# Kernel optimization log

Measured on AMD Instinct MI355X. Metric: run time of the kernel, lower is better.

## Reference

```python
import jax, jax.numpy as jnp
import numpy as np

NEG = -1e30  # safe -inf surrogate for log-space DP
BLANK = 0


def _ctc_loss_mean(log_probs, targets):
    """CTC loss matching torch.nn.functional.ctc_loss with reduction='mean',
    blank=0, full input lengths, and fixed target lengths L.
    log_probs: [T, B, C] (treated as log-probabilities, as F.ctc_loss does)
    targets:   [B, L] int labels in [1, C)
    """
    T, B, C = log_probs.shape
    L = targets.shape[1]
    S = 2 * L + 1  # extended label sequence: blank-interleaved

    # ext[b] = [blank, t1, blank, t2, blank]
    ext = jnp.zeros((B, S), dtype=targets.dtype).at[:, 1::2].set(targets)

    # lp_ext[t, b, s] = log_probs[t, b, ext[b, s]]
    lp_ext = jnp.take_along_axis(log_probs, jnp.broadcast_to(ext[None], (T, B, S)), axis=2)

    # transition s-2 -> s allowed only for non-blank states with distinct labels
    skip = jnp.concatenate(
        [jnp.zeros((B, 2), dtype=bool),
         (ext[:, 2:] != BLANK) & (ext[:, 2:] != ext[:, :-2])], axis=1)

    alpha0 = jnp.full((B, S), NEG, log_probs.dtype)
    alpha0 = alpha0.at[:, 0].set(lp_ext[0, :, 0]).at[:, 1].set(lp_ext[0, :, 1])

    neg1 = jnp.full((B, 1), NEG, log_probs.dtype)
    neg2 = jnp.full((B, 2), NEG, log_probs.dtype)

    def step(alpha, lp_t):
        p1 = jnp.concatenate([neg1, alpha[:, :-1]], axis=1)
        p2 = jnp.where(skip, jnp.concatenate([neg2, alpha[:, :-2]], axis=1), NEG)
        alpha_new = lp_t + jax.nn.logsumexp(jnp.stack([alpha, p1, p2]), axis=0)
        return alpha_new, None

    alphaT, _ = jax.lax.scan(step, alpha0, lp_ext[1:])  # scan over t = 1..T-1

    # path ends in last blank or last label
    log_lik = jax.nn.logsumexp(alphaT[:, S - 2:S], axis=1)  # [B]
    # torch 'mean': divide each loss by its target length, then batch mean
    return jnp.mean(-log_lik / L)


def setup_inputs() -> dict:
    T, B, C, L = 512, 32, 8000, 2
    key = jax.random.key(0)
    k1, k2, k3 = jax.random.split(key, 3)
    logit = jax.random.normal(k1, (T, B, C), dtype=jnp.float32)
    label = jax.random.randint(k2, (B, L), 0, C, dtype=jnp.int64)     # unused by forward
    targets = jax.random.randint(k3, (B, L), 1, 20, dtype=jnp.int64)  # torch.randint(1, 20, (B, 2))
    return {"logit": logit, "label": label, "targets": targets}


def reference(logit, label, targets):
    # The torch module ignores `label` and builds random length-2 targets;
    # we receive those as the deterministic `targets` input.
    return _ctc_loss_mean(logit, targets)
```

## Files before the change

kernel.cpp:

```cpp
#include <hip/hip_runtime.h>

#define TT 512
#define BB 32
#define CC 8000
#define LOG2E 1.4426950408889634f
#define LN2   0.6931471805599453f
#define NBLK  8

#if __has_builtin(__builtin_amdgcn_exp2f)
#define EXP2F(x) __builtin_amdgcn_exp2f(x)
#else
#define EXP2F(x) exp2f(x)
#endif
#if __has_builtin(__builtin_amdgcn_logf)
#define LOG2F(x) __builtin_amdgcn_logf(x)
#else
#define LOG2F(x) log2f(x)
#endif

#define WS_CNT_OFF (65 * 512 * 4)

__device__ __forceinline__ void triprod(const float a[15], const float b[15],
                                        float p[15]) {
    p[ 0] = a[0] * b[0];
    p[ 1] = fmaf(a[0], b[ 1], a[1] * b[ 5]);
    p[ 2] = fmaf(a[0], b[ 2], fmaf(a[1], b[ 6], a[2] * b[ 9]));
    p[ 3] = fmaf(a[0], b[ 3], fmaf(a[1], b[ 7], fmaf(a[2], b[10], a[3] * b[12])));
    p[ 4] = fmaf(a[0], b[ 4], fmaf(a[1], b[ 8], fmaf(a[2], b[11],
                 fmaf(a[3], b[13], a[4] * b[14]))));
    p[ 5] = a[5] * b[5];
    p[ 6] = fmaf(a[5], b[ 6], a[6] * b[ 9]);
    p[ 7] = fmaf(a[5], b[ 7], fmaf(a[6], b[10], a[7] * b[12]));
    p[ 8] = fmaf(a[5], b[ 8], fmaf(a[6], b[11], fmaf(a[7], b[13], a[8] * b[14])));
    p[ 9] = a[9] * b[9];
    p[10] = fmaf(a[9], b[10], a[10] * b[12]);
    p[11] = fmaf(a[9], b[11], fmaf(a[10], b[13], a[11] * b[14]));
    p[12] = a[12] * b[12];
    p[13] = fmaf(a[12], b[13], a[13] * b[14]);
    p[14] = a[14] * b[14];
}

__device__ __forceinline__ float renorm15(float p[15]) {
    float mx = p[0];
    #pragma unroll
    for (int i = 1; i < 15; ++i) mx = fmaxf(mx, p[i]);
    int ex = (int)((__float_as_uint(mx) >> 23) & 0xffu) - 127;
    float sc = __uint_as_float((unsigned)(127 - ex) << 23);
    #pragma unroll
    for (int i = 0; i < 15; ++i) p[i] *= sc;
    return (float)ex;
}

__global__ __launch_bounds__(256) void ctc_fused(
        const float* __restrict__ logit,
        const int* __restrict__ targets,
        float* __restrict__ ws,
        unsigned int* __restrict__ cnt,
        float* __restrict__ out) {
    __shared__ float lds[4 * 512];

    int tid = threadIdx.x;
    int bk  = blockIdx.x;
    int b   = tid & 31;
    int widx = tid >> 6;
    int c   = bk * 8 + (tid >> 5);
    int a1 = targets[2 * b];
    int a2 = targets[2 * b + 1];
    float skf = (a1 != a2) ? 1.0f : 0.0f;

    int tstart = (c == 0) ? 1 : 8 * c;
    int nst    = (c == 0) ? 7 : 8;

    float l0[8], la[8], lb[8];
    #pragma unroll
    for (int s = 0; s < 8; ++s) {
        const float* row = logit + (size_t)((tstart + s) * BB + b) * CC;
        l0[s] = row[0]  * LOG2E;
        la[s] = row[a1] * LOG2E;
        lb[s] = row[a2] * LOG2E;
    }

    float m0s = fmaxf(fmaxf(l0[0], la[0]), lb[0]);
    float P0 = EXP2F(l0[0] - m0s), Pa = EXP2F(la[0] - m0s), Pb = EXP2F(lb[0] - m0s);
    float Ec = m0s;
    float M00 = P0, M01 = Pa, M02 = 0.f, M03 = 0.f, M04 = 0.f;
    float M11 = Pa, M12 = P0, M13 = skf * Pb, M14 = 0.f;
    float M22 = P0, M23 = Pb, M24 = 0.f;
    float M33 = Pb, M34 = P0;
    float M44 = P0;

    #pragma unroll
    for (int s = 1; s < 8; ++s) {
        if (s >= nst) break;
        float ms = fmaxf(fmaxf(l0[s], la[s]), lb[s]);
        float q0 = EXP2F(l0[s] - ms);
        float qa = EXP2F(la[s] - ms);
        float qb = EXP2F(lb[s] - ms);
        Ec += ms;
        float n00 = M00 * q0;
        float n01 = (M00 + M01) * qa;
        float n02 = (M01 + M02) * q0;
        float n03 = fmaf(skf, M01, M02 + M03) * qb;
        float n04 = (M03 + M04) * q0;
        float n11 = M11 * qa;
        float n12 = (M11 + M12) * q0;
        float n13 = fmaf(skf, M11, M12 + M13) * qb;
        float n14 = (M13 + M14) * q0;
        float n22 = M22 * q0;
        float n23 = (M22 + M23) * qb;
        float n24 = (M23 + M24) * q0;
        float n33 = M33 * qb;
        float n34 = (M33 + M34) * q0;
        float n44 = M44 * q0;
        M00 = n00; M01 = n01; M02 = n02; M03 = n03; M04 = n04;
        M11 = n11; M12 = n12; M13 = n13; M14 = n14;
        M22 = n22; M23 = n23; M24 = n24;
        M33 = n33; M34 = n34;
        M44 = n44;
    }

    float lo[15] = {M00,M01,M02,M03,M04,M11,M12,M13,M14,M22,M23,M24,M33,M34,M44};

    float hi[15];
    #pragma unroll
    for (int i = 0; i < 15; ++i) hi[i] = __shfl_down(lo[i], 32, 64);
    float Ehi = __shfl_down(Ec, 32, 64);
    float pw[15];
    triprod(lo, hi, pw);
    float Ew = Ec + Ehi + renorm15(pw);

    if ((tid & 63) < 32) {
        float* d = lds + widx * 512 + b * 16;
        #pragma unroll
        for (int i = 0; i < 15; ++i) d[i] = pw[i];
        d[15] = Ew;
    }
    __syncthreads();
    if (tid >= 64) return;

    float w1[16], w2[16], w3[16];
    {
        const float* s1 = lds + 1 * 512 + b * 16;
        const float* s2 = lds + 2 * 512 + b * 16;
        const float* s3 = lds + 3 * 512 + b * 16;
        #pragma unroll
        for (int i = 0; i < 16; ++i) { w1[i] = s1[i]; w2[i] = s2[i]; w3[i] = s3[i]; }
    }
    float q1[15], q2[15], pf[15];
    triprod(pw, w1, q1);
    float E1 = Ew + w1[15] + renorm15(q1);
    triprod(w2, w3, q2);
    float E2 = w2[15] + w3[15] + renorm15(q2);
    triprod(q1, q2, pf);
    float Ef = E1 + E2 + renorm15(pf);

    int t1 = targets[2 * b];
    const float* row0 = logit + (size_t)b * CC;
    float l00 = row0[0] * LOG2E, la0 = row0[t1] * LOG2E;

    if (tid < 32) {
        float4* w = (float4*)(ws + (size_t)bk * 512 + b * 16);
        w[0] = make_float4(pf[ 0], pf[ 1], pf[ 2], pf[ 3]);
        w[1] = make_float4(pf[ 4], pf[ 5], pf[ 6], pf[ 7]);
        w[2] = make_float4(pf[ 8], pf[ 9], pf[10], pf[11]);
        w[3] = make_float4(pf[12], pf[13], pf[14], Ef);
    }

    __threadfence();
    unsigned int old = 0;
    if (tid == 0) old = atomicAdd(cnt, 1u);
    old = __shfl(old, 0, 64);
    if ((old & (NBLK - 1u)) != NBLK - 1u) return;
    __threadfence();

    float mi = fmaxf(l00, la0);
    float A0 = EXP2F(l00 - mi), A1 = EXP2F(la0 - mi);
    float A2 = 0.f, A3 = 0.f, A4 = 0.f;
    double Ed = (double)mi;
    int    Ei = 0;

    float4 mm[NBLK][4];
    #pragma unroll
    for (int k = 0; k < NBLK; ++k) {
        const float4* src = (const float4*)(ws + (size_t)k * 512 + b * 16);
        mm[k][0] = src[0]; mm[k][1] = src[1]; mm[k][2] = src[2]; mm[k][3] = src[3];
    }
    #pragma unroll
    for (int k = 0; k < NBLK; ++k) {
        float4 v0 = mm[k][0], v1 = mm[k][1], v2 = mm[k][2], v3 = mm[k][3];
        float B0 = A0 * v0.x;
        float B1 = fmaf(A0, v0.y, A1 * v1.y);
        float B2 = fmaf(A0, v0.z, fmaf(A1, v1.z, A2 * v2.y));
        float B3 = fmaf(A0, v0.w, fmaf(A1, v1.w, fmaf(A2, v2.z, A3 * v3.x)));
        float B4 = fmaf(A0, v1.x, fmaf(A1, v2.x, fmaf(A2, v2.w,
                        fmaf(A3, v3.y, A4 * v3.z))));
        Ed += (double)v3.w;
        float mx = fmaxf(fmaxf(fmaxf(B0, B1), fmaxf(B2, B3)), B4);
        int ex = (int)((__float_as_uint(mx) >> 23) & 0xffu) - 127;
        float sc = __uint_as_float((unsigned)(127 - ex) << 23);
        Ei += ex;
        A0 = B0 * sc; A1 = B1 * sc; A2 = B2 * sc; A3 = B3 * sc; A4 = B4 * sc;
    }

    float ll2 = (float)(Ed + (double)Ei) + LOG2F(A3 + A4);
    float loss = (tid < 32) ? (-0.5f * LN2 * ll2) : 0.0f;
    #pragma unroll
    for (int off = 32; off > 0; off >>= 1)
        loss += __shfl_down(loss, off, 64);
    if (tid == 0) out[0] = loss * (1.0f / BB);
}

extern "C" void kernel_launch(void* const* d_in, const int* in_sizes, int n_in,
                              void* d_out, int out_size, void* d_ws, size_t ws_size,
                              hipStream_t stream) {
    const float* logit   = (const float*)d_in[0];
    const int*   targets = (const int*)d_in[2];
    float*        ws  = (float*)d_ws;
    unsigned int* cnt = (unsigned int*)((char*)d_ws + WS_CNT_OFF);
    float*        out = (float*)d_out;

    hipLaunchKernelGGL(ctc_fused, dim3(NBLK), dim3(256), 0, stream,
                       logit, targets, ws, cnt, out);
}
```

Baseline: 11.90 us.

## Use cooperative grid sync with 32 single-wave blocks and tree combine

Replaces the 8-block, 256-thread kernel and its atomic-counter last-block reduction with 32 blocks of one wavefront each, launched cooperatively and joined by a grid-wide sync. Block 0 then combines the 32 partial transition matrices with a tree of triangular products split across two half-waves, instead of a serial 8-step chain. This spreads the gather loads over more CUs and shortens the serial combine. It adds the cost of a cooperative launch and grid barrier, which can carry more overhead than the atomic counter.

```diff
diff --git a/kernel.cpp b/kernel.cpp
--- a/kernel.cpp
+++ b/kernel.cpp
@@ -1,11 +1,14 @@
 #include <hip/hip_runtime.h>
+#include <hip/hip_cooperative_groups.h>
+
+namespace cg = cooperative_groups;
 
 #define TT 512
 #define BB 32
 #define CC 8000
 #define LOG2E 1.4426950408889634f
 #define LN2   0.6931471805599453f
-#define NBLK  8
+#define NBLK  32
 
 #if __has_builtin(__builtin_amdgcn_exp2f)
 #define EXP2F(x) __builtin_amdgcn_exp2f(x)
@@ -18,7 +21,6 @@
 #define LOG2F(x) log2f(x)
 #endif
 
-#define WS_CNT_OFF (65 * 512 * 4)
 
 __device__ __forceinline__ void triprod(const float a[15], const float b[15],
                                         float p[15]) {
@@ -51,19 +53,45 @@
     return (float)ex;
 }
 
-__global__ __launch_bounds__(256) void ctc_fused(
+#define COMBINE8(g, eg, base)                                                  \
+    {                                                                          \
+        float t8[8][15], e8[8];                                                \
+        _Pragma("unroll")                                                      \
+        for (int j = 0; j < 8; ++j) {                                          \
+            const float4* src =                                                \
+                (const float4*)(ws + (size_t)((base) + j) * 512 + b * 16);     \
+            float4 v0 = src[0], v1 = src[1], v2 = src[2], v3 = src[3];         \
+            t8[j][ 0] = v0.x; t8[j][ 1] = v0.y; t8[j][ 2] = v0.z;              \
+            t8[j][ 3] = v0.w; t8[j][ 4] = v1.x; t8[j][ 5] = v1.y;              \
+            t8[j][ 6] = v1.z; t8[j][ 7] = v1.w; t8[j][ 8] = v2.x;              \
+            t8[j][ 9] = v2.y; t8[j][10] = v2.z; t8[j][11] = v2.w;              \
+            t8[j][12] = v3.x; t8[j][13] = v3.y; t8[j][14] = v3.z;              \
+            e8[j] = v3.w;                                                      \
+        }                                                                      \
+        float p4[4][15], e4[4];                                                \
+        _Pragma("unroll")                                                      \
+        for (int j = 0; j < 4; ++j) {                                          \
+            triprod(t8[2 * j], t8[2 * j + 1], p4[j]);                          \
+            e4[j] = e8[2 * j] + e8[2 * j + 1] + renorm15(p4[j]);               \
+        }                                                                      \
+        float p2a[15], p2b[15];                                                \
+        triprod(p4[0], p4[1], p2a);                                            \
+        float e2a = e4[0] + e4[1] + renorm15(p2a);                             \
+        triprod(p4[2], p4[3], p2b);                                            \
+        float e2b = e4[2] + e4[3] + renorm15(p2b);                             \
+        triprod(p2a, p2b, g);                                                  \
+        eg = e2a + e2b + renorm15(g);                                          \
+    }
+
+__global__ __launch_bounds__(64, 1) void ctc_fused(
         const float* __restrict__ logit,
         const int* __restrict__ targets,
         float* __restrict__ ws,
-        unsigned int* __restrict__ cnt,
         float* __restrict__ out) {
-    __shared__ float lds[4 * 512];
-
     int tid = threadIdx.x;
     int bk  = blockIdx.x;
     int b   = tid & 31;
-    int widx = tid >> 6;
-    int c   = bk * 8 + (tid >> 5);
+    int c   = bk * 2 + (tid >> 5);
     int a1 = targets[2 * b];
     int a2 = targets[2 * b + 1];
     float skf = (a1 != a2) ? 1.0f : 0.0f;
@@ -79,6 +107,8 @@
         la[s] = row[a1] * LOG2E;
         lb[s] = row[a2] * LOG2E;
     }
+    const float* row0 = logit + (size_t)b * CC;
+    float l00 = row0[0] * LOG2E, la0 = row0[a1] * LOG2E;
 
     float m0s = fmaxf(fmaxf(l0[0], la[0]), lb[0]);
     float P0 = EXP2F(l0[0] - m0s), Pa = EXP2F(la[0] - m0s), Pb = EXP2F(lb[0] - m0s);
@@ -129,72 +159,44 @@
     triprod(lo, hi, pw);
     float Ew = Ec + Ehi + renorm15(pw);
 
-    if ((tid & 63) < 32) {
-        float* d = lds + widx * 512 + b * 16;
-        #pragma unroll
-        for (int i = 0; i < 15; ++i) d[i] = pw[i];
-        d[15] = Ew;
-    }
-    __syncthreads();
-    if (tid >= 64) return;
-
-    float w1[16], w2[16], w3[16];
-    {
-        const float* s1 = lds + 1 * 512 + b * 16;
-        const float* s2 = lds + 2 * 512 + b * 16;
-        const float* s3 = lds + 3 * 512 + b * 16;
-        #pragma unroll
-        for (int i = 0; i < 16; ++i) { w1[i] = s1[i]; w2[i] = s2[i]; w3[i] = s3[i]; }
-    }
-    float q1[15], q2[15], pf[15];
-    triprod(pw, w1, q1);
-    float E1 = Ew + w1[15] + renorm15(q1);
-    triprod(w2, w3, q2);
-    float E2 = w2[15] + w3[15] + renorm15(q2);
-    triprod(q1, q2, pf);
-    float Ef = E1 + E2 + renorm15(pf);
-
-    int t1 = targets[2 * b];
-    const float* row0 = logit + (size_t)b * CC;
-    float l00 = row0[0] * LOG2E, la0 = row0[t1] * LOG2E;
-
     if (tid < 32) {
         float4* w = (float4*)(ws + (size_t)bk * 512 + b * 16);
-        w[0] = make_float4(pf[ 0], pf[ 1], pf[ 2], pf[ 3]);
-        w[1] = make_float4(pf[ 4], pf[ 5], pf[ 6], pf[ 7]);
-        w[2] = make_float4(pf[ 8], pf[ 9], pf[10], pf[11]);
-        w[3] = make_float4(pf[12], pf[13], pf[14], Ef);
-    }
-
-    __threadfence();
-    unsigned int old = 0;
-    if (tid == 0) old = atomicAdd(cnt, 1u);
-    old = __shfl(old, 0, 64);
-    if ((old & (NBLK - 1u)) != NBLK - 1u) return;
-    __threadfence();
+        w[0] = make_float4(pw[ 0], pw[ 1], pw[ 2], pw[ 3]);
+        w[1] = make_float4(pw[ 4], pw[ 5], pw[ 6], pw[ 7]);
+        w[2] = make_float4(pw[ 8], pw[ 9], pw[10], pw[11]);
+        w[3] = make_float4(pw[12], pw[13], pw[14], Ew);
+    }
+
+    cg::this_grid().sync();
+    if (bk != 0) return;
+
+    int base = (tid >> 5) * 16;
+    float g0[15], g1[15];
+    float eg0, eg1;
+    COMBINE8(g0, eg0, base)
+    COMBINE8(g1, eg1, base + 8)
+    float halfp[15];
+    triprod(g0, g1, halfp);
+    float ehalf = eg0 + eg1 + renorm15(halfp);
+
+    float hih[15];
+    #pragma unroll
+    for (int i = 0; i < 15; ++i) hih[i] = __shfl_down(halfp[i], 32, 64);
+    float ehi2 = __shfl_down(ehalf, 32, 64);
 
     float mi = fmaxf(l00, la0);
     float A0 = EXP2F(l00 - mi), A1 = EXP2F(la0 - mi);
     float A2 = 0.f, A3 = 0.f, A4 = 0.f;
-    double Ed = (double)mi;
-    int    Ei = 0;
-
-    float4 mm[NBLK][4];
-    #pragma unroll
-    for (int k = 0; k < NBLK; ++k) {
-        const float4* src = (const float4*)(ws + (size_t)k * 512 + b * 16);
-        mm[k][0] = src[0]; mm[k][1] = src[1]; mm[k][2] = src[2]; mm[k][3] = src[3];
-    }
-    #pragma unroll
-    for (int k = 0; k < NBLK; ++k) {
-        float4 v0 = mm[k][0], v1 = mm[k][1], v2 = mm[k][2], v3 = mm[k][3];
-        float B0 = A0 * v0.x;
-        float B1 = fmaf(A0, v0.y, A1 * v1.y);
-        float B2 = fmaf(A0, v0.z, fmaf(A1, v1.z, A2 * v2.y));
-        float B3 = fmaf(A0, v0.w, fmaf(A1, v1.w, fmaf(A2, v2.z, A3 * v3.x)));
-        float B4 = fmaf(A0, v1.x, fmaf(A1, v2.x, fmaf(A2, v2.w,
-                        fmaf(A3, v3.y, A4 * v3.z))));
-        Ed += (double)v3.w;
+    int Ei = 0;
+    #pragma unroll
+    for (int k = 0; k < 2; ++k) {
+        const float* m = (k == 0) ? halfp : hih;
+        float B0 = A0 * m[0];
+        float B1 = fmaf(A0, m[1], A1 * m[5]);
+        float B2 = fmaf(A0, m[2], fmaf(A1, m[6], A2 * m[9]));
+        float B3 = fmaf(A0, m[3], fmaf(A1, m[7], fmaf(A2, m[10], A3 * m[12])));
+        float B4 = fmaf(A0, m[4], fmaf(A1, m[8], fmaf(A2, m[11],
+                        fmaf(A3, m[13], A4 * m[14]))));
         float mx = fmaxf(fmaxf(fmaxf(B0, B1), fmaxf(B2, B3)), B4);
         int ex = (int)((__float_as_uint(mx) >> 23) & 0xffu) - 127;
         float sc = __uint_as_float((unsigned)(127 - ex) << 23);
@@ -202,7 +204,8 @@
         A0 = B0 * sc; A1 = B1 * sc; A2 = B2 * sc; A3 = B3 * sc; A4 = B4 * sc;
     }
 
-    float ll2 = (float)(Ed + (double)Ei) + LOG2F(A3 + A4);
+    double Ed = (double)mi + (double)ehalf + (double)ehi2 + (double)Ei;
+    float ll2 = (float)Ed + LOG2F(A3 + A4);
     float loss = (tid < 32) ? (-0.5f * LN2 * ll2) : 0.0f;
     #pragma unroll
     for (int off = 32; off > 0; off >>= 1)
@@ -215,10 +218,10 @@
                               hipStream_t stream) {
     const float* logit   = (const float*)d_in[0];
     const int*   targets = (const int*)d_in[2];
-    float*        ws  = (float*)d_ws;
-    unsigned int* cnt = (unsigned int*)((char*)d_ws + WS_CNT_OFF);
-    float*        out = (float*)d_out;
-
-    hipLaunchKernelGGL(ctc_fused, dim3(NBLK), dim3(256), 0, stream,
-                       logit, targets, ws, cnt, out);
-}
+    float*       ws      = (float*)d_ws;
+    float*       out     = (float*)d_out;
+
+    void* args[] = {(void*)&logit, (void*)&targets, (void*)&ws, (void*)&out};
+    hipLaunchCooperativeKernel((const void*)ctc_fused, dim3(NBLK), dim3(64),
+                               args, 0, stream);
+}
```

New measurement: 36.80 us. +209.3%, slower.
